# Optimization experiments

Measured on AMD Instinct MI355X. Metric: run time of the kernel, lower is better.

Reference implementation:

```python
import jax, jax.numpy as jnp
import numpy as np
import itertools

N_OBJECTS = 6  # subsets of range(6), sizes 1..6 -> 63 subsets

def _subset_groups():
    # group subsets by length so each group runs as one batched LSTM
    groups = {}
    for m in range(1, N_OBJECTS + 1):
        for s in itertools.combinations(range(6), m):
            groups.setdefault(m, []).append(list(s))
    return [(m, np.asarray(v, dtype=np.int32)) for m, v in groups.items()]

SUBSET_GROUPS = _subset_groups()


def _lstm_final_h(x, W_ih, W_hh, b_ih, b_hh):
    """x: [B,T,D] -> final hidden state [B,H]. PyTorch gate order i,f,g,o."""
    H = W_hh.shape[1]
    B = x.shape[0]
    # precompute input projections for all timesteps: [B,T,4H]
    xz = jnp.einsum('btd,gd->btg', x, W_ih) + b_ih + b_hh

    def step(carry, xt):
        h, c = carry
        z = xt + h @ W_hh.T
        i, f, g, o = jnp.split(z, 4, axis=-1)
        c = jax.nn.sigmoid(f) * c + jax.nn.sigmoid(i) * jnp.tanh(g)
        h = jax.nn.sigmoid(o) * jnp.tanh(c)
        return (h, c), None

    h0 = jnp.zeros((B, H), x.dtype)
    (h, _), _ = jax.lax.scan(step, (h0, h0), jnp.swapaxes(xz, 0, 1))
    return h


def setup_inputs() -> dict:
    key = jax.random.key(0)
    ks = jax.random.split(key, 10)
    D, H, FC, A = 16, 128, 256, 10
    mb = 8192
    s = lambda k, shape, fan: jax.random.normal(k, shape, jnp.float32) * (1.0 / np.sqrt(fan))
    return {
        'x_input': jax.random.normal(ks[0], (mb, 6, D), jnp.float32),
        'W_ih': s(ks[1], (4 * H, D), D),
        'W_hh': s(ks[2], (4 * H, H), H),
        'b_ih': jnp.zeros((4 * H,), jnp.float32),
        'b_hh': jnp.zeros((4 * H,), jnp.float32),
        'fc1_W': s(ks[3], (FC, H), H),
        'fc1_b': jnp.zeros((FC,), jnp.float32),
        'fc2_W': s(ks[4], (A, FC), FC),
        'fc2_b': jnp.zeros((A,), jnp.float32),
    }


def reference(x_input, W_ih, W_hh, b_ih, b_hh, fc1_W, fc1_b, fc2_W, fc2_b):
    mb = x_input.shape[0]
    H = W_hh.shape[1]
    hs = []
    # subsets of the same length are batched into one LSTM pass (fused form of
    # the original 63-iteration python loop); aggregation is permutation-invariant
    for m, idx in SUBSET_GROUPS:
        nL = idx.shape[0]
        xg = x_input[:, idx, :]                       # [mb, nL, m, D] gather
        xg = xg.reshape(mb * nL, m, x_input.shape[-1])
        h = _lstm_final_h(xg, W_ih, W_hh, b_ih, b_hh)  # [mb*nL, H]
        hs.append(h.reshape(mb, nL, H))
    holder = jnp.concatenate(hs, axis=1)              # [mb, 63, H]
    x = jnp.max(holder, axis=1)                       # aggregate == 'max'
    x = jax.nn.relu(x @ fc1_W.T + fc1_b)
    x = x @ fc2_W.T + fc2_b
    return jax.nn.log_softmax(x, axis=-1)
```

## Files before the change

kernel.cpp:

```cpp
#include <hip/hip_runtime.h>
#include <hip/hip_bf16.h>

#define BLOCK   1024
#define NSAMP   16
#define HDIM    128
#define DDIM    16
#define NOBJ    6
#define NSLOT   16

typedef __attribute__((ext_vector_type(8))) short bf16x8;
typedef __attribute__((ext_vector_type(4))) float f32x4;

constexpr int pc6(int m)  { int c = 0; for (int i = 0; i < 6; ++i) c += (m >> i) & 1; return c; }
constexpr int msb6(int m) { int b = -1; for (int i = 0; i < 6; ++i) if (m & (1 << i)) b = i; return b; }

struct NodeRec { int jo, ps, sl; };
struct Plan { int cnt[7]; int n1[7]; NodeRec nd[7][20]; };
constexpr Plan make_plan() {
    Plan P{};
    int slotOf[64] = {};
    bool busy[NSLOT] = {};
    for (int d = 1; d <= 6; ++d) {
        int n = 0;
        for (int M = 1; M < 64; ++M) {
            if (pc6(M) != d || msb6(M) != 5) continue;
            P.nd[d][n].jo = 5;
            P.nd[d][n].ps = (d == 1) ? -1 : slotOf[M & ~(1 << 5)];
            P.nd[d][n].sl = -1;
            ++n;
        }
        int pend[20] = {}; int np = 0;
        for (int M = 1; M < 64; ++M) {
            if (pc6(M) != d || msb6(M) >= 5) continue;
            const int hi = msb6(M);
            int fs = -1;
            for (int s = 0; s < NSLOT; ++s) if (!busy[s]) { fs = s; break; }
            if (fs >= 0) {
                busy[fs] = true; slotOf[M] = fs;
                P.nd[d][n].jo = hi;
                P.nd[d][n].ps = (d == 1) ? -1 : slotOf[M & ~(1 << hi)];
                P.nd[d][n].sl = fs;
                ++n;
            } else pend[np++] = M;
        }
        P.n1[d] = n;
        int freeds[20] = {}; int nf = 0;
        if (d >= 2)
            for (int M = 1; M < 64; ++M)
                if (pc6(M) == d - 1 && msb6(M) == 4) freeds[nf++] = slotOf[M];
        for (int i = 0; i < np; ++i) {
            const int M = pend[i]; const int hi = msb6(M);
            const int s = freeds[--nf];
            slotOf[M] = s;
            P.nd[d][n].jo = hi;
            P.nd[d][n].ps = slotOf[M & ~(1 << hi)];
            P.nd[d][n].sl = s;
            ++n;
        }
        P.cnt[d] = n;
        for (int s = 0; s < NSLOT; ++s) busy[s] = false;
        for (int M = 1; M < 64; ++M)
            if (pc6(M) == d && msb6(M) < 5) busy[slotOf[M]] = true;
    }
    return P;
}
constexpr Plan PL = make_plan();

#define LOG2E   1.44269504f
#define TWOL2E  2.88539008f
#define SLOT_SH (16 * NSAMP * 8)

__device__ __forceinline__ float fast_sig(float z) {
    float e = __builtin_amdgcn_exp2f(-LOG2E * z);
    return __builtin_amdgcn_rcpf(1.0f + e);
}
__device__ __forceinline__ float fast_tanh(float z) {
    float e = __builtin_amdgcn_exp2f(TWOL2E * z);
    float r = __builtin_amdgcn_rcpf(1.0f + e);
    return fmaf(-2.0f, r, 1.0f);
}
__device__ __forceinline__ unsigned short f2bf(float x) {
    union { float f; unsigned int u; } a; a.f = x;
    unsigned int r = (a.u + 0x7FFFu + ((a.u >> 16) & 1u)) >> 16;
    return (unsigned short)r;
}


__global__ __launch_bounds__(BLOCK)
void subset_lstm_w16_kernel(
    const float* __restrict__ x_input,
    const float* __restrict__ W_ih,
    const float* __restrict__ W_hh,
    const float* __restrict__ b_ih,
    const float* __restrict__ b_hh,
    const float* __restrict__ fc1_W,
    const float* __restrict__ fc1_b,
    const float* __restrict__ fc2_W,
    const float* __restrict__ fc2_b,
    float* __restrict__ out)
{
    __shared__ __align__(16) unsigned short hs[NSLOT * SLOT_SH];
    __shared__ __align__(16) unsigned short xb[NOBJ * 2 * NSAMP * 8];
    __shared__ __align__(16) unsigned short xpad[16];
    float* s_maxh  = (float*)hs;
    float* s_fc1   = (float*)(hs + 4096);
    float* s_logit = (float*)xb;

    const int t      = threadIdx.x;
    const int w      = t >> 6;
    const int lane   = t & 63;
    const int quad   = lane >> 4;
    const int m16    = lane & 15;
    const int cb     = w * 8;
    const int s_base = blockIdx.x * NSAMP;

    if (t < 16) xpad[t] = (t == 0) ? f2bf(1.0f) : (unsigned short)0;

    for (int idx = t; idx < NOBJ * 2 * NSAMP * 8; idx += BLOCK) {
        const int j = idx & 7, n = (idx >> 3) & 15, q = (idx >> 7) & 1, obj = idx >> 8;
        xb[idx] = f2bf(x_input[(s_base + n) * (NOBJ * DDIM) + obj * DDIM + q * 8 + j]);
    }

    bf16x8 wf[2][5];
    #pragma unroll
    for (int T = 0; T < 2; ++T) {
        const int chan = cb + (m16 >> 1);
        const int gate = 2 * T + (m16 & 1);
        const int grow = gate * HDIM + chan;
        const float* whr = W_hh + grow * HDIM;
        const float* wir = W_ih + grow * DDIM;
        #pragma unroll
        for (int q = 0; q < 4; ++q) {
            union { unsigned short u[8]; bf16x8 v; } pk;
            #pragma unroll
            for (int j = 0; j < 8; ++j)
                pk.u[j] = f2bf(whr[q * 32 + quad * 8 + j]);
            wf[T][q] = pk.v;
        }
        {
            union { unsigned short u[8]; bf16x8 v; } pk;
            #pragma unroll
            for (int j = 0; j < 8; ++j) {
                float v = 0.0f;
                if (quad < 2) v = wir[quad * 8 + j];
                else if (quad == 2 && j == 0) v = b_ih[grow] + b_hh[grow];
                pk.u[j] = f2bf(v);
            }
            wf[T][4] = pk.v;
        }
    }

    float cs[NSLOT][2];
    float mh0 = -1e30f, mh1 = -1e30f;

    #pragma unroll
    for (int d = 1; d <= 6; ++d) {
        __syncthreads();
        #pragma unroll
        for (int ni = 0; ni < PL.cnt[d]; ++ni) {
            if (ni == PL.n1[d]) __syncthreads();
            const int jo = PL.nd[d][ni].jo;
            const int ps = PL.nd[d][ni].ps;
            const int sl = PL.nd[d][ni].sl;

            f32x4 aIF = f32x4{0.f, 0.f, 0.f, 0.f};
            f32x4 aGO = f32x4{0.f, 0.f, 0.f, 0.f};

            {
                const unsigned short* bp = (quad < 2)
                    ? &xb[((jo * 2 + quad) * NSAMP + m16) * 8]
                    : &xpad[(quad - 2) * 8];
                const bf16x8 bfx = *(const bf16x8*)bp;
                aIF = __builtin_amdgcn_mfma_f32_16x16x32_bf16(wf[0][4], bfx, aIF, 0, 0, 0);
                aGO = __builtin_amdgcn_mfma_f32_16x16x32_bf16(wf[1][4], bfx, aGO, 0, 0, 0);
            }
            if (ps >= 0) {
                #pragma unroll
                for (int q = 0; q < 4; ++q) {
                    const bf16x8 bh = *(const bf16x8*)
                        &hs[ps * SLOT_SH + (((q * 4 + quad) * NSAMP) + m16) * 8];
                    aIF = __builtin_amdgcn_mfma_f32_16x16x32_bf16(wf[0][q], bh, aIF, 0, 0, 0);
                    aGO = __builtin_amdgcn_mfma_f32_16x16x32_bf16(wf[1][q], bh, aGO, 0, 0, 0);
                }
            }

            float hnv[2];
            #pragma unroll
            for (int u = 0; u < 2; ++u) {
                const float zi = aIF[2 * u], zf = aIF[2 * u + 1];
                const float zg = aGO[2 * u], zo = aGO[2 * u + 1];
                const float cprev = (ps >= 0) ? cs[ps][u] : 0.0f;
                const float ig = fast_sig(zi);
                const float fg = fast_sig(zf);
                const float gg = fast_tanh(zg);
                const float og = fast_sig(zo);
                const float cn = fmaf(fg, cprev, ig * gg);
                const float h  = og * fast_tanh(cn);
                hnv[u] = h;
                if (sl >= 0) cs[sl][u] = cn;
            }
            mh0 = fmaxf(mh0, hnv[0]);
            mh1 = fmaxf(mh1, hnv[1]);

            if (sl >= 0) {
                const __hip_bfloat162 hp = __float22bfloat162_rn(float2{hnv[0], hnv[1]});
                *(__hip_bfloat162*)&hs[sl * SLOT_SH + ((w * NSAMP) + m16) * 8 + 2 * quad] = hp;
            }
        }
    }

    __syncthreads();
    {
        float2 v; v.x = mh0; v.y = mh1;
        *(float2*)&s_maxh[m16 * HDIM + cb + 2 * quad] = v;
    }
    __syncthreads();

    {
        const int f  = t & 255;
        const int sh = t >> 8;
        float a1[4];
        #pragma unroll
        for (int s = 0; s < 4; ++s) a1[s] = fc1_b[f];
        for (int k4 = 0; k4 < HDIM / 4; ++k4) {
            const float4 wv = *(const float4*)&fc1_W[f * HDIM + k4 * 4];
            #pragma unroll
            for (int s = 0; s < 4; ++s) {
                const float4 h4 = *(const float4*)&s_maxh[(sh * 4 + s) * HDIM + k4 * 4];
                a1[s] += wv.x * h4.x + wv.y * h4.y + wv.z * h4.z + wv.w * h4.w;
            }
        }
        #pragma unroll
        for (int s = 0; s < 4; ++s)
            s_fc1[(sh * 4 + s) * 256 + f] = fmaxf(a1[s], 0.0f);
    }
    __syncthreads();

    if (t < NSAMP * 10) {
        const int s = t / 10, a = t % 10;
        float acc2 = fc2_b[a];
        for (int f4 = 0; f4 < 256 / 4; ++f4) {
            const float4 wv = *(const float4*)&fc2_W[a * 256 + f4 * 4];
            const float4 v  = *(const float4*)&s_fc1[s * 256 + f4 * 4];
            acc2 += wv.x * v.x + wv.y * v.y + wv.z * v.z + wv.w * v.w;
        }
        s_logit[s * 10 + a] = acc2;
    }
    __syncthreads();

    if (t < NSAMP) {
        float m = -1e30f;
        #pragma unroll
        for (int a = 0; a < 10; ++a) m = fmaxf(m, s_logit[t * 10 + a]);
        float sum = 0.0f;
        #pragma unroll
        for (int a = 0; a < 10; ++a) sum += __expf(s_logit[t * 10 + a] - m);
        const float lse = m + __logf(sum);
        #pragma unroll
        for (int a = 0; a < 10; ++a)
            out[(s_base + t) * 10 + a] = s_logit[t * 10 + a] - lse;
    }
}

extern "C" void kernel_launch(void* const* d_in, const int* in_sizes, int n_in,
                              void* d_out, int out_size, void* d_ws, size_t ws_size,
                              hipStream_t stream)
{
    (void)d_ws; (void)ws_size; (void)n_in; (void)out_size;

    const float* x   = (const float*)d_in[0];
    const float* Wih = (const float*)d_in[1];
    const float* Whh = (const float*)d_in[2];
    const float* bih = (const float*)d_in[3];
    const float* bhh = (const float*)d_in[4];
    const float* f1w = (const float*)d_in[5];
    const float* f1b = (const float*)d_in[6];
    const float* f2w = (const float*)d_in[7];
    const float* f2b = (const float*)d_in[8];

    const int mb = in_sizes[0] / (NOBJ * DDIM);
    dim3 grid(mb / NSAMP), block(BLOCK);
    subset_lstm_w16_kernel<<<grid, block, 0, stream>>>(
        x, Wih, Whh, bih, bhh, f1w, f1b, f2w, f2b, (float*)d_out);
}
```

Baseline: 218.0 us.

## Process 32 samples per 512-thread block with all four gates per warp

Each wave now owns 16 hidden channels across all four gates and two 16-sample subtiles, so every LDS B-fragment load of h feeds four MFMAs. Block size halves to 512 threads with 32 samples per block, and launch bounds request two blocks per CU. The cell state is stored packed as bf16 in registers to save register space, at the cost of cell-state precision. Register pressure rises from 20 weight fragments and 8 accumulators per lane, which may spill or limit occupancy.

```diff
diff --git a/kernel.cpp b/kernel.cpp
--- a/kernel.cpp
+++ b/kernel.cpp
@@ -1,8 +1,8 @@
 #include <hip/hip_runtime.h>
 #include <hip/hip_bf16.h>
 
-#define BLOCK   1024
-#define NSAMP   16
+#define BLOCK   512
+#define NSAMP   32
 #define HDIM    128
 #define DDIM    16
 #define NOBJ    6
@@ -84,10 +84,21 @@
     unsigned int r = (a.u + 0x7FFFu + ((a.u >> 16) & 1u)) >> 16;
     return (unsigned short)r;
 }
-
-
-__global__ __launch_bounds__(BLOCK)
-void subset_lstm_w16_kernel(
+__device__ __forceinline__ unsigned pk2(float a, float b) {
+    union { __hip_bfloat162 h; unsigned u; } z;
+    z.h = __float22bfloat162_rn(float2{a, b});
+    return z.u;
+}
+__device__ __forceinline__ float bflo(unsigned p) {
+    union { unsigned u; float f; } a; a.u = p << 16; return a.f;
+}
+__device__ __forceinline__ float bfhi(unsigned p) {
+    union { unsigned u; float f; } a; a.u = p & 0xFFFF0000u; return a.f;
+}
+
+
+__global__ __launch_bounds__(BLOCK, 2)
+void subset_lstm_n32_kernel(
     const float* __restrict__ x_input,
     const float* __restrict__ W_ih,
     const float* __restrict__ W_hh,
@@ -103,7 +114,7 @@
     __shared__ __align__(16) unsigned short xb[NOBJ * 2 * NSAMP * 8];
     __shared__ __align__(16) unsigned short xpad[16];
     float* s_maxh  = (float*)hs;
-    float* s_fc1   = (float*)(hs + 4096);
+    float* s_fc1   = (float*)(hs + 8192);
     float* s_logit = (float*)xb;
 
     const int t      = threadIdx.x;
@@ -111,22 +122,19 @@
     const int lane   = t & 63;
     const int quad   = lane >> 4;
     const int m16    = lane & 15;
-    const int cb     = w * 8;
     const int s_base = blockIdx.x * NSAMP;
 
     if (t < 16) xpad[t] = (t == 0) ? f2bf(1.0f) : (unsigned short)0;
 
     for (int idx = t; idx < NOBJ * 2 * NSAMP * 8; idx += BLOCK) {
-        const int j = idx & 7, n = (idx >> 3) & 15, q = (idx >> 7) & 1, obj = idx >> 8;
+        const int j = idx & 7, n = (idx >> 3) & 31, q = (idx >> 8) & 1, obj = idx >> 9;
         xb[idx] = f2bf(x_input[(s_base + n) * (NOBJ * DDIM) + obj * DDIM + q * 8 + j]);
     }
 
-    bf16x8 wf[2][5];
+    bf16x8 wf[4][5];
     #pragma unroll
-    for (int T = 0; T < 2; ++T) {
-        const int chan = cb + (m16 >> 1);
-        const int gate = 2 * T + (m16 & 1);
-        const int grow = gate * HDIM + chan;
+    for (int g = 0; g < 4; ++g) {
+        const int grow = g * HDIM + w * 16 + m16;
         const float* whr = W_hh + grow * HDIM;
         const float* wir = W_ih + grow * DDIM;
         #pragma unroll
@@ -135,7 +143,7 @@
             #pragma unroll
             for (int j = 0; j < 8; ++j)
                 pk.u[j] = f2bf(whr[q * 32 + quad * 8 + j]);
-            wf[T][q] = pk.v;
+            wf[g][q] = pk.v;
         }
         {
             union { unsigned short u[8]; bf16x8 v; } pk;
@@ -146,12 +154,18 @@
                 else if (quad == 2 && j == 0) v = b_ih[grow] + b_hh[grow];
                 pk.u[j] = f2bf(v);
             }
-            wf[T][4] = pk.v;
-        }
-    }
-
-    float cs[NSLOT][2];
-    float mh0 = -1e30f, mh1 = -1e30f;
+            wf[g][4] = pk.v;
+        }
+    }
+
+    uint2 cs[NSLOT][2];
+    float mh[2][4];
+    #pragma unroll
+    for (int st = 0; st < 2; ++st)
+        #pragma unroll
+        for (int r = 0; r < 4; ++r) mh[st][r] = -1e30f;
+
+    const int kslot = w * 2 + (quad >> 1);
 
     #pragma unroll
     for (int d = 1; d <= 6; ++d) {
@@ -163,76 +177,95 @@
             const int ps = PL.nd[d][ni].ps;
             const int sl = PL.nd[d][ni].sl;
 
-            f32x4 aIF = f32x4{0.f, 0.f, 0.f, 0.f};
-            f32x4 aGO = f32x4{0.f, 0.f, 0.f, 0.f};
-
-            {
+            f32x4 acc[4][2];
+            #pragma unroll
+            for (int g = 0; g < 4; ++g)
+                #pragma unroll
+                for (int st = 0; st < 2; ++st)
+                    acc[g][st] = f32x4{0.f, 0.f, 0.f, 0.f};
+
+            #pragma unroll
+            for (int st = 0; st < 2; ++st) {
                 const unsigned short* bp = (quad < 2)
-                    ? &xb[((jo * 2 + quad) * NSAMP + m16) * 8]
+                    ? &xb[((jo * 2 + quad) * NSAMP + st * 16 + m16) * 8]
                     : &xpad[(quad - 2) * 8];
                 const bf16x8 bfx = *(const bf16x8*)bp;
-                aIF = __builtin_amdgcn_mfma_f32_16x16x32_bf16(wf[0][4], bfx, aIF, 0, 0, 0);
-                aGO = __builtin_amdgcn_mfma_f32_16x16x32_bf16(wf[1][4], bfx, aGO, 0, 0, 0);
+                #pragma unroll
+                for (int g = 0; g < 4; ++g)
+                    acc[g][st] = __builtin_amdgcn_mfma_f32_16x16x32_bf16(
+                        wf[g][4], bfx, acc[g][st], 0, 0, 0);
             }
             if (ps >= 0) {
                 #pragma unroll
-                for (int q = 0; q < 4; ++q) {
-                    const bf16x8 bh = *(const bf16x8*)
-                        &hs[ps * SLOT_SH + (((q * 4 + quad) * NSAMP) + m16) * 8];
-                    aIF = __builtin_amdgcn_mfma_f32_16x16x32_bf16(wf[0][q], bh, aIF, 0, 0, 0);
-                    aGO = __builtin_amdgcn_mfma_f32_16x16x32_bf16(wf[1][q], bh, aGO, 0, 0, 0);
+                for (int q = 0; q < 4; ++q)
+                    #pragma unroll
+                    for (int st = 0; st < 2; ++st) {
+                        const bf16x8 bh = *(const bf16x8*)
+                            &hs[((ps * 16 + q * 4 + quad) * NSAMP + st * 16 + m16) * 8];
+                        #pragma unroll
+                        for (int g = 0; g < 4; ++g)
+                            acc[g][st] = __builtin_amdgcn_mfma_f32_16x16x32_bf16(
+                                wf[g][q], bh, acc[g][st], 0, 0, 0);
+                    }
+            }
+
+            #pragma unroll
+            for (int st = 0; st < 2; ++st) {
+                float cn4[4], hn4[4];
+                #pragma unroll
+                for (int r = 0; r < 4; ++r) {
+                    float cprev = 0.0f;
+                    if (ps >= 0) {
+                        const unsigned p = (r < 2) ? cs[ps][st].x : cs[ps][st].y;
+                        cprev = (r & 1) ? bfhi(p) : bflo(p);
+                    }
+                    const float ig = fast_sig(acc[0][st][r]);
+                    const float fg = fast_sig(acc[1][st][r]);
+                    const float gg = fast_tanh(acc[2][st][r]);
+                    const float og = fast_sig(acc[3][st][r]);
+                    const float cn = fmaf(fg, cprev, ig * gg);
+                    const float h  = og * fast_tanh(cn);
+                    cn4[r] = cn; hn4[r] = h;
+                    mh[st][r] = fmaxf(mh[st][r], h);
                 }
-            }
-
-            float hnv[2];
-            #pragma unroll
-            for (int u = 0; u < 2; ++u) {
-                const float zi = aIF[2 * u], zf = aIF[2 * u + 1];
-                const float zg = aGO[2 * u], zo = aGO[2 * u + 1];
-                const float cprev = (ps >= 0) ? cs[ps][u] : 0.0f;
-                const float ig = fast_sig(zi);
-                const float fg = fast_sig(zf);
-                const float gg = fast_tanh(zg);
-                const float og = fast_sig(zo);
-                const float cn = fmaf(fg, cprev, ig * gg);
-                const float h  = og * fast_tanh(cn);
-                hnv[u] = h;
-                if (sl >= 0) cs[sl][u] = cn;
-            }
-            mh0 = fmaxf(mh0, hnv[0]);
-            mh1 = fmaxf(mh1, hnv[1]);
-
-            if (sl >= 0) {
-                const __hip_bfloat162 hp = __float22bfloat162_rn(float2{hnv[0], hnv[1]});
-                *(__hip_bfloat162*)&hs[sl * SLOT_SH + ((w * NSAMP) + m16) * 8 + 2 * quad] = hp;
+                if (sl >= 0) {
+                    cs[sl][st].x = pk2(cn4[0], cn4[1]);
+                    cs[sl][st].y = pk2(cn4[2], cn4[3]);
+                    union { __hip_bfloat162 h2[2]; uint2 v; } hp;
+                    hp.h2[0] = __float22bfloat162_rn(float2{hn4[0], hn4[1]});
+                    hp.h2[1] = __float22bfloat162_rn(float2{hn4[2], hn4[3]});
+                    *(uint2*)&hs[((sl * 16 + kslot) * NSAMP + st * 16 + m16) * 8
+                                 + (quad & 1) * 4] = hp.v;
+                }
             }
         }
     }
 
     __syncthreads();
-    {
-        float2 v; v.x = mh0; v.y = mh1;
-        *(float2*)&s_maxh[m16 * HDIM + cb + 2 * quad] = v;
+    #pragma unroll
+    for (int st = 0; st < 2; ++st) {
+        float4 v; v.x = mh[st][0]; v.y = mh[st][1]; v.z = mh[st][2]; v.w = mh[st][3];
+        *(float4*)&s_maxh[(st * 16 + m16) * HDIM + w * 16 + quad * 4] = v;
     }
     __syncthreads();
 
     {
         const int f  = t & 255;
         const int sh = t >> 8;
-        float a1[4];
-        #pragma unroll
-        for (int s = 0; s < 4; ++s) a1[s] = fc1_b[f];
+        float a1[16];
+        #pragma unroll
+        for (int s = 0; s < 16; ++s) a1[s] = fc1_b[f];
         for (int k4 = 0; k4 < HDIM / 4; ++k4) {
             const float4 wv = *(const float4*)&fc1_W[f * HDIM + k4 * 4];
             #pragma unroll
-            for (int s = 0; s < 4; ++s) {
-                const float4 h4 = *(const float4*)&s_maxh[(sh * 4 + s) * HDIM + k4 * 4];
+            for (int s = 0; s < 16; ++s) {
+                const float4 h4 = *(const float4*)&s_maxh[(sh * 16 + s) * HDIM + k4 * 4];
                 a1[s] += wv.x * h4.x + wv.y * h4.y + wv.z * h4.z + wv.w * h4.w;
             }
         }
         #pragma unroll
-        for (int s = 0; s < 4; ++s)
-            s_fc1[(sh * 4 + s) * 256 + f] = fmaxf(a1[s], 0.0f);
+        for (int s = 0; s < 16; ++s)
+            s_fc1[(sh * 16 + s) * 256 + f] = fmaxf(a1[s], 0.0f);
     }
     __syncthreads();
 
@@ -280,6 +313,6 @@
 
     const int mb = in_sizes[0] / (NOBJ * DDIM);
     dim3 grid(mb / NSAMP), block(BLOCK);
-    subset_lstm_w16_kernel<<<grid, block, 0, stream>>>(
+    subset_lstm_n32_kernel<<<grid, block, 0, stream>>>(
         x, Wih, Whh, bih, bhh, f1w, f1b, f2w, f2b, (float*)d_out);
 }
```

After: 221.3 us. No clear change (+1.5%).
